# Kernel tuning notes

Measured on AMD Instinct MI355X. Metric: run time of the kernel, lower is better.

Reference implementation:

```python
import jax, jax.numpy as jnp
import numpy as np

B, T, IN = 32, 64, 90
U, SEG = 4, 16          # conductor steps, decoder steps per segment (T = U*SEG)
H1, HC, HD, Z = 2048, 1024, 1024, 512


def _lstm_layer(x, wih, whh, bih, bhh, h0=None, c0=None, reverse=False):
    """PyTorch-convention LSTM layer. x: [B,T,D]. Returns (ys [B,T,H], final h [B,H])."""
    b = x.shape[0]
    H = whh.shape[1]
    # precompute input projection for all timesteps: [T,B,4H]
    xp = jnp.swapaxes(jnp.einsum('btd,gd->btg', x, wih) + bih, 0, 1)
    if h0 is None:
        h0 = jnp.zeros((b, H), x.dtype)
        c0 = h0
    def step(carry, xt):
        h, c = carry
        g = xt + h @ whh.T + bhh
        i, f, gg, o = jnp.split(g, 4, axis=-1)  # torch gate order i,f,g,o
        c = jax.nn.sigmoid(f) * c + jax.nn.sigmoid(i) * jnp.tanh(gg)
        h = jax.nn.sigmoid(o) * jnp.tanh(c)
        return (h, c), h
    (h, c), ys = jax.lax.scan(step, (h0, c0), xp, reverse=reverse)
    return jnp.swapaxes(ys, 0, 1), h


def _cell(xin, h, c, wih, whh, bih, bhh):
    g = xin @ wih.T + bih + h @ whh.T + bhh
    i, f, gg, o = jnp.split(g, 4, axis=-1)
    c = jax.nn.sigmoid(f) * c + jax.nn.sigmoid(i) * jnp.tanh(gg)
    h = jax.nn.sigmoid(o) * jnp.tanh(c)
    return h, c


def setup_inputs() -> dict:
    key = jax.random.key(0)
    ks = iter(jax.random.split(key, 64))
    def p(*shape):
        return jax.random.normal(next(ks), shape, dtype=jnp.float32) * 0.02
    inp = {}
    inp['x'] = jax.random.normal(next(ks), (B, T, IN), dtype=jnp.float32)
    inp['eps'] = jax.random.normal(next(ks), (B, Z), dtype=jnp.float32)
    # encoder bi-LSTM: 2 layers x 2 directions
    for name, d in [('e0f', IN), ('e0b', IN), ('e1f', 2 * H1), ('e1b', 2 * H1)]:
        inp[name + '_wih'] = p(4 * H1, d)
        inp[name + '_whh'] = p(4 * H1, H1)
        inp[name + '_bih'] = p(4 * H1)
        inp[name + '_bhh'] = p(4 * H1)
    inp['wm'] = p(Z, 2 * H1); inp['bm'] = p(Z)
    inp['ws'] = p(Z, 2 * H1); inp['bs'] = p(Z)
    inp['w2'] = p(4 * HC, Z); inp['b2'] = p(4 * HC)
    # conductor LSTM: 2 layers, input size 1
    for name, d in [('c0', 1), ('c1', HC)]:
        inp[name + '_wih'] = p(4 * HC, d)
        inp[name + '_whh'] = p(4 * HC, HC)
        inp[name + '_bih'] = p(4 * HC)
        inp[name + '_bhh'] = p(4 * HC)
    inp['w3'] = p(4 * HD, HC); inp['b3'] = p(4 * HD)
    # two decoder LSTMCells
    for name, d in [('d1', HC + IN), ('d2', HD)]:
        inp[name + '_wih'] = p(4 * HD, d)
        inp[name + '_whh'] = p(4 * HD, HD)
        inp[name + '_bih'] = p(4 * HD)
        inp[name + '_bhh'] = p(4 * HD)
    inp['w4'] = p(IN, HD); inp['b4'] = p(IN)
    return inp


def reference(x, eps,
              e0f_wih, e0f_whh, e0f_bih, e0f_bhh,
              e0b_wih, e0b_whh, e0b_bih, e0b_bhh,
              e1f_wih, e1f_whh, e1f_bih, e1f_bhh,
              e1b_wih, e1b_whh, e1b_bih, e1b_bhh,
              wm, bm, ws, bs, w2, b2,
              c0_wih, c0_whh, c0_bih, c0_bhh,
              c1_wih, c1_whh, c1_bih, c1_bhh,
              w3, b3,
              d1_wih, d1_whh, d1_bih, d1_bhh,
              d2_wih, d2_whh, d2_bih, d2_bhh,
              w4, b4):
    b = x.shape[0]
    # ----- encode: 2-layer bidirectional LSTM, take layer-1 fwd/bwd final h -----
    y0f, _ = _lstm_layer(x, e0f_wih, e0f_whh, e0f_bih, e0f_bhh)
    y0b, _ = _lstm_layer(x, e0b_wih, e0b_whh, e0b_bih, e0b_bhh, reverse=True)
    y0 = jnp.concatenate([y0f, y0b], axis=2)  # [B,T,2*H1]
    _, hf = _lstm_layer(y0, e1f_wih, e1f_whh, e1f_bih, e1f_bhh)
    _, hb = _lstm_layer(y0, e1b_wih, e1b_whh, e1b_bih, e1b_bhh, reverse=True)
    ht = jnp.concatenate([hf, hb], axis=1)  # [B,4096]
    z_mean = ht @ wm.T + bm
    z_std = jnp.log1p(jnp.exp(ht @ ws.T + bs))  # softplus as in source
    z = z_mean + eps * z_std
    # ----- conductor -----
    t = jnp.tanh(z @ w2.T + b2)
    h1, h2, c1, c2 = jnp.split(t, 4, axis=1)  # source order: h1,h2,c1,c2
    zin = jnp.zeros((b, U, 1), x.dtype)
    yc0, _ = _lstm_layer(zin, c0_wih, c0_whh, c0_bih, c0_bhh, h1, c1)
    emb, _ = _lstm_layer(yc0, c1_wih, c1_whh, c1_bih, c1_bhh, h2, c2)  # [B,U,HC]
    def segment(prev, e):
        s = jnp.tanh(e @ w3.T + b3)
        sh1, sh2, sc1, sc2 = jnp.split(s, 4, axis=1)
        def step(carry, _):
            dh1, dc1, dh2, dc2, p = carry
            inp = jnp.concatenate([e, p], axis=1)
            dh1, dc1 = _cell(inp, dh1, dc1, d1_wih, d1_whh, d1_bih, d1_bhh)
            dh2, dc2 = _cell(dh1, dh2, dc2, d2_wih, d2_whh, d2_bih, d2_bhh)
            p = dh2 @ w4.T + b4
            return (dh1, dc1, dh2, dc2, p), p
        carry, outs = jax.lax.scan(step, (sh1, sc1, sh2, sc2, prev), None, length=SEG)
        return carry[4], outs  # outs: [SEG,B,IN]
    prev0 = jnp.zeros((b, IN), x.dtype)
    _, outs = jax.lax.scan(segment, prev0, jnp.swapaxes(emb, 0, 1))  # [U,SEG,B,IN]
    out = jnp.transpose(outs.reshape(U * SEG, b, IN), (1, 0, 2))  # [B,T,IN]
    out = jax.nn.softmax(out, axis=2)
    return out, z_mean, z_std
```

## Files before the change

kernel.cpp:

```cpp
#include <hip/hip_runtime.h>
#include <hip/hip_cooperative_groups.h>
#include <math.h>

#define BB 32
#define TT 64
#define INPW 90
#define NU 4
#define NH1 2048
#define NHC 1024
#define NHD 1024
#define NZ 512
#define BSTRIDE 12800

typedef unsigned short u16;
typedef __attribute__((ext_vector_type(8))) short short8;
typedef __attribute__((ext_vector_type(4))) float f32x4;
typedef __attribute__((ext_vector_type(4))) unsigned uv4;
typedef __attribute__((ext_vector_type(2))) unsigned uv2;

__device__ __forceinline__ float sigf(float v) { return 1.0f / (1.0f + __expf(-v)); }

__device__ __forceinline__ u16 f2bf(float f) {
  unsigned u = __float_as_uint(f);
  unsigned r = (u + 0x7FFFu + ((u >> 16) & 1u)) >> 16;
  return (u16)r;
}
__device__ __forceinline__ float bf2f(u16 b) { return __uint_as_float(((unsigned)b) << 16); }

__device__ __forceinline__ void cstore16(u16* p, uv4 v) {
  asm volatile("global_store_dwordx4 %0, %1, off sc0 sc1" :: "v"(p), "v"(v) : "memory");
}
__device__ __forceinline__ void cstore8(u16* p, uv2 v) {
  asm volatile("global_store_dwordx2 %0, %1, off sc0 sc1" :: "v"(p), "v"(v) : "memory");
}
__device__ __forceinline__ void cstore4(unsigned* p, unsigned v) {
  asm volatile("global_store_dword %0, %1, off sc0 sc1" :: "v"(p), "v"(v) : "memory");
}
__device__ __forceinline__ unsigned fload(const unsigned* p) {
  unsigned r;
  asm volatile("global_load_dword %0, %1, off sc0 sc1\n\ts_waitcnt vmcnt(0)"
               : "=v"(r) : "v"(p) : "memory");
  return r;
}
__device__ __forceinline__ void gbar(unsigned* base) {
  asm volatile("s_waitcnt vmcnt(0)" ::: "memory");
  __syncthreads();
  if (threadIdx.x == 0) {
    unsigned old = atomicAdd(&base[(blockIdx.x & 15) * 512], 1u);
    if (old == 15u) {
      unsigned m = atomicAdd(&base[16 * 512], 1u);
      if (m == 15u) {
#pragma unroll
        for (int k = 0; k < 8; ++k) cstore4(&base[(17 + k) * 512], 1u);
        asm volatile("s_waitcnt vmcnt(0)" ::: "memory");
      }
    }
    while (!fload(&base[(17 + (blockIdx.x & 7)) * 512])) __builtin_amdgcn_s_sleep(2);
  }
  __syncthreads();
}

__global__ void cvt_flat(const float* __restrict__ s, u16* __restrict__ d, long n) {
  long i = ((long)blockIdx.x * 256 + threadIdx.x) * 4;
  if (i >= n) return;
  float4 v = *(const float4*)&s[i];
  d[i] = f2bf(v.x); d[i + 1] = f2bf(v.y); d[i + 2] = f2bf(v.z); d[i + 3] = f2bf(v.w);
}

__global__ void cvt_pad(const float* __restrict__ s, int sld, int cols,
                        u16* __restrict__ d, int dld, int rows) {
  int c = blockIdx.x * blockDim.x + threadIdx.x;
  int r = blockIdx.y;
  if (c >= dld) return;
  d[(long)r * dld + c] = (c < cols) ? f2bf(s[(long)r * sld + c]) : (u16)0;
}

__global__ void xcvt(const float* __restrict__ x, u16* __restrict__ xb) {
  int r = blockIdx.x, c = threadIdx.x;
  int b = r & 31, t = r >> 5;
  float v = (c < INPW) ? x[((long)b * TT + t) * INPW + c] : 0.0f;
  xb[(long)r * 128 + c] = f2bf(v);
}

__global__ void w4t_k(const float* __restrict__ w4, u16* __restrict__ w4tb) {
  int k = blockIdx.x, n = threadIdx.x;
  w4tb[(long)k * 128 + n] = (n < INPW) ? f2bf(w4[(long)n * NHD + k]) : (u16)0;
}

__global__ void bfuse_k(const float* __restrict__ d1_wih, const float* __restrict__ b4,
                        float* __restrict__ bfuse) {
  int r = blockIdx.x * 256 + threadIdx.x;
  if (r >= 4096) return;
  float s = 0.0f;
  for (int n = 0; n < INPW; ++n) s += d1_wih[(long)r * 1114 + 1024 + n] * b4[n];
  bfuse[r] = s;
}

__global__ __launch_bounds__(256) void gemm_bf(
    const u16* __restrict__ A, int lda, const u16* __restrict__ Bw, int ldb,
    const float* __restrict__ bias, u16* __restrict__ C, int ldc, int K, int mode,
    int nbm, int nbn) {
  __shared__ u16 Asm[128 * 64];
  __shared__ u16 Bsm[128 * 64];
  const int tid = threadIdx.x;
  const int w = tid >> 6, q = (tid >> 4) & 3, ln = tid & 15;
  const int wm = w & 1, wn = w >> 1;
  int fid = blockIdx.x;
  int sidx = fid >> 3, xcd = fid & 7;
  int bm, bn;
  if ((nbm & 7) == 0) { bn = sidx % nbn; bm = xcd * (nbm >> 3) + sidx / nbn; }
  else if ((nbn & 7) == 0) { bm = sidx % nbm; bn = xcd * (nbn >> 3) + sidx / nbm; }
  else { bm = fid % nbm; bn = fid / nbm; }
  const long am0 = (long)bm * 128;
  const long bn0 = (long)bn * 128;
  f32x4 acc[4][4] = {};
  const int srow = tid >> 3, ssl = tid & 7;
  const u16* Ap = A + (am0 + srow) * lda + ssl * 8;
  const u16* Bp = Bw + (bn0 + srow) * ldb + ssl * 8;
  uint4 va[4], vb[4];
  int soff[4];
#pragma unroll
  for (int i = 0; i < 4; ++i) {
    va[i] = *(const uint4*)(Ap + (long)i * 32 * lda);
    vb[i] = *(const uint4*)(Bp + (long)i * 32 * ldb);
    int r = srow + i * 32;
    soff[i] = r * 64 + ((ssl ^ (r & 7)) << 3);
  }
  int k0 = 0;
  for (;;) {
    __syncthreads();
#pragma unroll
    for (int i = 0; i < 4; ++i) {
      *(uint4*)&Asm[soff[i]] = va[i];
      *(uint4*)&Bsm[soff[i]] = vb[i];
    }
    __syncthreads();
    k0 += 64;
    if (k0 < K) {
#pragma unroll
      for (int i = 0; i < 4; ++i) {
        va[i] = *(const uint4*)(Ap + k0 + (long)i * 32 * lda);
        vb[i] = *(const uint4*)(Bp + k0 + (long)i * 32 * ldb);
      }
    }
#pragma unroll
    for (int kh = 0; kh < 2; ++kh) {
      short8 af[4], bg[4];
#pragma unroll
      for (int t = 0; t < 4; ++t) {
        int arr = wm * 64 + t * 16 + ln;
        af[t] = *(short8*)&Asm[arr * 64 + (((q + 4 * kh) ^ (arr & 7)) << 3)];
        int brr = wn * 64 + t * 16 + ln;
        bg[t] = *(short8*)&Bsm[brr * 64 + (((q + 4 * kh) ^ (brr & 7)) << 3)];
      }
#pragma unroll
      for (int mt = 0; mt < 4; ++mt)
#pragma unroll
        for (int nt = 0; nt < 4; ++nt)
          acc[mt][nt] = __builtin_amdgcn_mfma_f32_16x16x32_bf16(af[mt], bg[nt], acc[mt][nt], 0, 0, 0);
    }
    if (k0 >= K) break;
  }
#pragma unroll
  for (int nt = 0; nt < 4; ++nt) {
    long n = bn0 + wn * 64 + nt * 16 + ln;
    float bv = bias ? bias[n] : 0.0f;
#pragma unroll
    for (int mt = 0; mt < 4; ++mt) {
#pragma unroll
      for (int r = 0; r < 4; ++r) {
        long m = am0 + wm * 64 + mt * 16 + (q << 2) + r;
        long dst;
        if (mode == 0) {
          dst = m * ldc + n;
        } else if (mode == 1) {
          long j = n & 2047, g = n >> 11;
          dst = (((m >> 5) * 256 + (j >> 3)) * 32 + (m & 31)) * 32 + (j & 7) * 4 + g;
        } else {
          long j = n & 1023, g = n >> 10;
          dst = ((j >> 2) * 128 + m) * 16 + (j & 3) * 4 + g;
        }
        C[dst] = f2bf(acc[mt][nt][r] + bv);
      }
    }
  }
}

__global__ __launch_bounds__(256) void gemm128(
    const float* __restrict__ A, int lda, const float* __restrict__ W, int ldw,
    const float* __restrict__ bias, float* __restrict__ C, int ldc,
    int M, int K, int act, u16* __restrict__ Cb) {
  __shared__ float As[16][132];
  __shared__ float Bs[16][132];
  const int tid = threadIdx.x;
  const int bm = blockIdx.x, bn = blockIdx.y;
  const int tm = tid & 15, tn = tid >> 4;
  float acc[8][8] = {};
  for (int k0 = 0; k0 < K; k0 += 16) {
#pragma unroll
    for (int it = 0; it < 2; ++it) {
      int e = it * 256 + tid;
      int r = e >> 2, c4 = (e & 3) * 4;
      int m = bm * 128 + r;
      float4 v = make_float4(0.f, 0.f, 0.f, 0.f);
      if (m < M) v = *(const float4*)&A[(long)m * lda + k0 + c4];
      As[c4 + 0][r] = v.x; As[c4 + 1][r] = v.y; As[c4 + 2][r] = v.z; As[c4 + 3][r] = v.w;
      int n = bn * 128 + r;
      float4 w = *(const float4*)&W[(long)n * ldw + k0 + c4];
      Bs[c4 + 0][r] = w.x; Bs[c4 + 1][r] = w.y; Bs[c4 + 2][r] = w.z; Bs[c4 + 3][r] = w.w;
    }
    __syncthreads();
#pragma unroll
    for (int kk = 0; kk < 16; ++kk) {
      float4 a0 = *(const float4*)&As[kk][tm * 8];
      float4 a1 = *(const float4*)&As[kk][tm * 8 + 4];
      float4 b0 = *(const float4*)&Bs[kk][tn * 8];
      float4 b1 = *(const float4*)&Bs[kk][tn * 8 + 4];
      float av[8] = {a0.x, a0.y, a0.z, a0.w, a1.x, a1.y, a1.z, a1.w};
      float bv[8] = {b0.x, b0.y, b0.z, b0.w, b1.x, b1.y, b1.z, b1.w};
#pragma unroll
      for (int i = 0; i < 8; ++i)
#pragma unroll
        for (int j = 0; j < 8; ++j)
          acc[i][j] += av[i] * bv[j];
    }
    __syncthreads();
  }
#pragma unroll
  for (int i = 0; i < 8; ++i) {
    int m = bm * 128 + tm * 8 + i;
    if (m >= M) continue;
#pragma unroll
    for (int j = 0; j < 8; ++j) {
      int n = bn * 128 + tn * 8 + j;
      float v = acc[i][j] + bias[n];
      if (act == 1) v = tanhf(v);
      else if (act == 2) v = log1pf(__expf(v));
      C[(long)m * ldc + n] = v;
      if (Cb) Cb[(long)m * ldc + n] = f2bf(v);
    }
  }
}

__global__ __launch_bounds__(256) void latgemm(
    const float* __restrict__ A, const float* __restrict__ W,
    const float* __restrict__ bias, float* __restrict__ C, int act) {
  __shared__ float red[16][16][32];
  const int tid = threadIdx.x;
  const int c = tid & 15, ksl = tid >> 4;
  const int n = blockIdx.x * 16 + c;
  const float* wp = W + (long)n * 4096 + ksl * 256;
  const float* ap = A + ksl * 256;
  float acc[32];
#pragma unroll
  for (int r = 0; r < 32; ++r) acc[r] = 0.f;
  for (int k = 0; k < 256; k += 4) {
    float4 wv = *(const float4*)(wp + k);
#pragma unroll
    for (int r = 0; r < 32; ++r) {
      float4 hv = *(const float4*)(ap + (long)r * 4096 + k);
      acc[r] += hv.x * wv.x + hv.y * wv.y + hv.z * wv.z + hv.w * wv.w;
    }
  }
#pragma unroll
  for (int r = 0; r < 32; ++r) red[ksl][c][r] = acc[r];
  __syncthreads();
  for (int o = tid; o < 512; o += 256) {
    int cc = o >> 5, r = o & 31;
    float s = 0.f;
#pragma unroll
    for (int p = 0; p < 16; ++p) s += red[p][cc][r];
    s += bias[blockIdx.x * 16 + cc];
    if (act == 2) s = log1pf(__expf(s));
    C[(long)r * 512 + blockIdx.x * 16 + cc] = s;
  }
}

__global__ void zcalc_kernel(const float* __restrict__ zm, const float* __restrict__ zs,
                             const float* __restrict__ eps, float* __restrict__ z) {
  int e = blockIdx.x * 256 + threadIdx.x;
  if (e < BB * NZ) z[e] = zm[e] + eps[e] * zs[e];
}

__global__ void softmax_kernel(float* __restrict__ out) {
  long row = blockIdx.x;
  float* p = out + row * INPW;
  int lane = threadIdx.x;
  float v0 = (lane < INPW) ? p[lane] : -1e30f;
  float v1 = (lane + 64 < INPW) ? p[lane + 64] : -1e30f;
  float m = fmaxf(v0, v1);
#pragma unroll
  for (int off = 32; off > 0; off >>= 1) m = fmaxf(m, __shfl_xor(m, off));
  float e0 = (lane < INPW) ? __expf(v0 - m) : 0.0f;
  float e1 = (lane + 64 < INPW) ? __expf(v1 - m) : 0.0f;
  float sum = e0 + e1;
#pragma unroll
  for (int off = 32; off > 0; off >>= 1) sum += __shfl_xor(sum, off);
  float inv = 1.0f / sum;
  if (lane < INPW) p[lane] = e0 * inv;
  if (lane + 64 < INPW) p[lane + 64] = e1 * inv;
}

struct EncArgs {
  const u16* whh[2];
  const u16* xp[2];
  const float* bhh[2];
  u16* y0b;
  u16* h1a[2];
  float* htb;
  unsigned* bar;
  int layer;
};

__global__ __launch_bounds__(512) void enc_coop(EncArgs A) {
  __shared__ u16 Wl[2 * 64 * 64 * 8];
  __shared__ __align__(16) float red[4 * 64 * 4];
  __shared__ __align__(16) u16 hstage[32][8];
  const int tid = threadIdx.x;
  const int w = tid >> 6, l = tid & 63;
  const int rt = w & 1, bh = (w >> 1) & 1, kh = w >> 2;
  const int kg = l >> 4, b0 = l & 15;
  const int j0 = blockIdx.x * 8;
  const int jout = j0 + rt * 4 + kg;
  const int batch = bh * 16 + b0;
  float* redp = &red[((bh * 2 + rt) * 64 + l) * 4];

  for (int dir = 0; dir < 2; ++dir) {
    __syncthreads();
    {
      const u16* W = A.whh[dir];
      for (int e = tid; e < 8192; e += 512) {
        int ert = e >> 12, es = (e >> 6) & 63, el = e & 63;
        int etr = el & 15;
        long gr = (long)(etr & 3) * 2048 + j0 + ert * 4 + (etr >> 2);
        *(uint4*)&Wl[((ert * 64 + es) * 64 + el) * 8] =
            *(const uint4*)&W[gr * 2048 + (el >> 4) * 8 + (long)es * 32];
      }
    }
    __syncthreads();
    const float* bhh = A.bhh[dir];
    const u16* xp = A.xp[dir];
    const float bi0 = bhh[jout], bi1 = bhh[2048 + jout],
                bi2 = bhh[4096 + jout], bi3 = bhh[6144 + jout];
    float creg = 0.f;
    ushort4 xv4 = make_ushort4(0, 0, 0, 0);
    if (kh == 0) {
      int tt0 = dir ? 63 : 0;
      xv4 = *(const ushort4*)(xp + ((((long)tt0 * 256 + blockIdx.x) * 32 + batch) * 32)
                              + (rt * 4 + kg) * 4);
    }
    for (int s = 0; s < 64; ++s) {
      if (s) gbar(A.bar + (long)(dir * 63 + (s - 1)) * BSTRIDE);
      const int tt = dir ? 63 - s : s;
      f32x4 acc = {0.f, 0.f, 0.f, 0.f};
      if (s) {
        const u16* hb; long hld;
        if (A.layer == 0) {
          int tp = dir ? tt + 1 : tt - 1;
          hb = A.y0b + (long)tp * 32 * 4096 + dir * 2048;
          hld = 4096;
        } else {
          hb = A.h1a[dir] + (long)(s - 1) * 32 * 2048;
          hld = 2048;
        }
        const u16* xv = hb + (long)batch * hld + kg * 8;
        for (int ks = kh * 32; ks < kh * 32 + 32; ks += 8) {
          uint4 bv[8]; short8 av[8];
#pragma unroll
          for (int uu = 0; uu < 8; ++uu)
            bv[uu] = *(const uint4*)(xv + (long)(ks + uu) * 32);
#pragma unroll
          for (int uu = 0; uu < 8; ++uu)
            av[uu] = *(const short8*)&Wl[((rt * 64 + ks + uu) * 64 + l) * 8];
#pragma unroll
          for (int uu = 0; uu < 8; ++uu)
            acc = __builtin_amdgcn_mfma_f32_16x16x32_bf16(av[uu], *(short8*)&bv[uu], acc, 0, 0, 0);
        }
      }
      if (kh) *(f32x4*)redp = acc;
      __syncthreads();
      if (kh == 0) {
        f32x4 o = *(f32x4*)redp;
        float g0 = acc[0] + o[0] + bi0 + bf2f(xv4.x);
        float g1 = acc[1] + o[1] + bi1 + bf2f(xv4.y);
        float g2 = acc[2] + o[2] + bi2 + bf2f(xv4.z);
        float g3 = acc[3] + o[3] + bi3 + bf2f(xv4.w);
        float iv = sigf(g0), fv = sigf(g1), gv = tanhf(g2), ov = sigf(g3);
        float c = fv * creg + iv * gv;
        creg = c;
        float h = ov * tanhf(c);
        hstage[batch][rt * 4 + kg] = f2bf(h);
        if (A.layer == 1 && s == 63) A.htb[batch * 4096 + dir * 2048 + jout] = h;
      }
      __syncthreads();
      if (tid < 32) {
        uv4 v = *(const uv4*)&hstage[tid][0];
        u16* dst;
        if (A.layer == 0) dst = &A.y0b[((long)tt * 32 + tid) * 4096 + dir * 2048 + j0];
        else dst = &A.h1a[dir][((long)s * 32 + tid) * 2048 + j0];
        cstore16(dst, v);
      }
      if (kh == 0 && s < 63) {
        int ttn = dir ? 62 - s : s + 1;
        xv4 = *(const ushort4*)(xp + ((((long)ttn * 256 + blockIdx.x) * 32 + batch) * 32)
                                + (rt * 4 + kg) * 4);
      }
    }
  }
}

__device__ __forceinline__ void stage_w1024(u16* Wl, int m, const u16* W, int j0, int tid) {
  for (int e = tid; e < 2048; e += 512) {
    int kh = e >> 10, s = (e >> 6) & 15, el = e & 63;
    int tr = el & 15;
    long gr = (long)(tr & 3) * 1024 + j0 + (tr >> 2);
    *(uint4*)&Wl[(((m * 2 + kh) * 16 + s) * 64 + el) * 8] =
        *(const uint4*)&W[gr * 1024 + kh * 512 + (el >> 4) * 8 + s * 32];
  }
}

__device__ __forceinline__ void cell1024_lds(
    const u16* Wl, int m0, int m1,
    int j0, int tid, float* red, u16* hstage,
    const u16* X0, long x0ld,
    const u16* X1, long x1ld,
    float xg0, float xg1, float xg2, float xg3,
    float b0, float b1, float b2, float b3,
    float co, float* crp,
    u16* hout, long hld, float* houtf, long hfld) {
  const int w = tid >> 6, l = tid & 63;
  const int bh = w & 1, kh = w >> 1;
  const int kg = l >> 4;
  const int koff = kh * 256 + kg * 8;
  const int batch = bh * 16 + (l & 15);
  const int sbase = (kh >> 1) * 16 + (kh & 1) * 8;
  const int jout = j0 + kg;
  f32x4 acc = {0.f, 0.f, 0.f, 0.f};
  if (X0) {
    const u16* xpt = X0 + (long)batch * x0ld + koff;
    const int sb = m0 * 32 + sbase;
    uint4 bv[8]; short8 av[8];
#pragma unroll
    for (int uu = 0; uu < 8; ++uu) bv[uu] = *(const uint4*)(xpt + (long)uu * 32);
#pragma unroll
    for (int uu = 0; uu < 8; ++uu) av[uu] = *(const short8*)&Wl[((sb + uu) * 64 + l) * 8];
#pragma unroll
    for (int uu = 0; uu < 8; ++uu)
      acc = __builtin_amdgcn_mfma_f32_16x16x32_bf16(av[uu], *(short8*)&bv[uu], acc, 0, 0, 0);
  }
  if (X1) {
    const u16* xpt = X1 + (long)batch * x1ld + koff;
    const int sb = m1 * 32 + sbase;
    uint4 bv[8]; short8 av[8];
#pragma unroll
    for (int uu = 0; uu < 8; ++uu) bv[uu] = *(const uint4*)(xpt + (long)uu * 32);
#pragma unroll
    for (int uu = 0; uu < 8; ++uu) av[uu] = *(const short8*)&Wl[((sb + uu) * 64 + l) * 8];
#pragma unroll
    for (int uu = 0; uu < 8; ++uu)
      acc = __builtin_amdgcn_mfma_f32_16x16x32_bf16(av[uu], *(short8*)&bv[uu], acc, 0, 0, 0);
  }
  if (kh) *(f32x4*)&red[((kh - 1) * 2 + bh) * 256 + l * 4] = acc;
  __syncthreads();
  if (kh == 0) {
#pragma unroll
    for (int p = 0; p < 3; ++p) {
      f32x4 o = *(f32x4*)&red[(p * 2 + bh) * 256 + l * 4];
      acc[0] += o[0]; acc[1] += o[1]; acc[2] += o[2]; acc[3] += o[3];
    }
    float g0 = acc[0] + b0 + xg0;
    float g1 = acc[1] + b1 + xg1;
    float g2 = acc[2] + b2 + xg2;
    float g3 = acc[3] + b3 + xg3;
    float iv = sigf(g0), fv = sigf(g1), gv = tanhf(g2), ov = sigf(g3);
    float c = fv * co + iv * gv;
    *crp = c;
    float h = ov * tanhf(c);
    hstage[batch * 4 + kg] = f2bf(h);
    if (houtf) houtf[(long)batch * hfld + jout] = h;
  }
  __syncthreads();
  if (tid < 32) {
    uv2 v = *(const uv2*)&hstage[tid * 4];
    cstore8(&hout[(long)tid * hld + j0], v);
  }
}

struct CondArgs {
  const u16 *c0h, *c1w, *c1h, *tvecb;
  const float* tvec;
  u16 *yc0b, *embb;
  float* embf;
  const float *b0i, *b0h, *b1i, *b1h;
  unsigned* bar;
};
__global__ __launch_bounds__(512) void cond_coop(CondArgs A) {
  __shared__ u16 Wl[3 * 32 * 512];
  __shared__ __align__(16) float red[6 * 256];
  __shared__ __align__(16) u16 hstage[128];
  const int j0 = blockIdx.x * 4;
  const int tid = threadIdx.x;
  const int w = tid >> 6, l = tid & 63;
  const int bh = w & 1;
  const int jout = j0 + (l >> 4);
  const int batch = bh * 16 + (l & 15);
  stage_w1024(Wl, 0, A.c0h, j0, tid);
  stage_w1024(Wl, 1, A.c1w, j0, tid);
  stage_w1024(Wl, 2, A.c1h, j0, tid);
  const float cb00 = A.b0i[jout] + A.b0h[jout];
  const float cb01 = A.b0i[1024 + jout] + A.b0h[1024 + jout];
  const float cb02 = A.b0i[2048 + jout] + A.b0h[2048 + jout];
  const float cb03 = A.b0i[3072 + jout] + A.b0h[3072 + jout];
  const float cb10 = A.b1i[jout] + A.b1h[jout];
  const float cb11 = A.b1i[1024 + jout] + A.b1h[1024 + jout];
  const float cb12 = A.b1i[2048 + jout] + A.b1h[2048 + jout];
  const float cb13 = A.b1i[3072 + jout] + A.b1h[3072 + jout];
  const float c0init = A.tvec[2048 + (long)batch * 4096 + jout];
  const float c1init = A.tvec[3072 + (long)batch * 4096 + jout];
  __syncthreads();
  float cr0 = c0init, cr1 = c1init;
  int bi = 0;
  for (int u = 0; u < NU; ++u) {
    cell1024_lds(Wl, 0, -1, j0, tid, red, hstage,
                 u ? A.yc0b + (long)(u - 1) * 32 * 1024 : A.tvecb, u ? 1024 : 4096,
                 nullptr, 0,
                 0.f, 0.f, 0.f, 0.f,
                 cb00, cb01, cb02, cb03,
                 cr0, &cr0,
                 A.yc0b + (long)u * 32 * 1024, 1024, nullptr, 0);
    gbar(A.bar + (long)(bi++) * BSTRIDE);
    cell1024_lds(Wl, 1, 2, j0, tid, red, hstage,
                 A.yc0b + (long)u * 32 * 1024, 1024,
                 u ? A.embb + (long)(u - 1) * 32 * 1024 : A.tvecb + 1024, u ? 1024 : 4096,
                 0.f, 0.f, 0.f, 0.f,
                 cb10, cb11, cb12, cb13,
                 cr1, &cr1,
                 A.embb + (long)u * 32 * 1024, 1024, A.embf + (long)u * 32 * 1024, 1024);
    if (u < NU - 1) gbar(A.bar + (long)(bi++) * BSTRIDE);
  }
}

struct DecArgs {
  const u16 *d1h, *wfuse, *d2w, *d2h, *xeb, *sallb;
  const float* sall;
  u16 *dh1all, *dh2all;
  const float *bfuse, *b1h, *b2i, *b2h;
  unsigned* bar;
};
__global__ __launch_bounds__(512) void dec_coop(DecArgs A) {
  __shared__ u16 Wl[4 * 32 * 512];
  __shared__ __align__(16) float red[6 * 256];
  __shared__ __align__(16) u16 hstage[128];
  const int j0 = blockIdx.x * 4;
  const int tid = threadIdx.x;
  const int w = tid >> 6, l = tid & 63;
  const int bh = w & 1;
  const int kg = l >> 4;
  const int jout = j0 + kg;
  const int batch = bh * 16 + (l & 15);
  stage_w1024(Wl, 0, A.d1h, j0, tid);
  stage_w1024(Wl, 1, A.wfuse, j0, tid);
  stage_w1024(Wl, 2, A.d2w, j0, tid);
  stage_w1024(Wl, 3, A.d2h, j0, tid);
  const float b1z0 = A.b1h[jout], b1z1 = A.b1h[1024 + jout],
              b1z2 = A.b1h[2048 + jout], b1z3 = A.b1h[3072 + jout];
  const float b1n0 = b1z0 + A.bfuse[jout], b1n1 = b1z1 + A.bfuse[1024 + jout],
              b1n2 = b1z2 + A.bfuse[2048 + jout], b1n3 = b1z3 + A.bfuse[3072 + jout];
  const float b20 = A.b2i[jout] + A.b2h[jout];
  const float b21 = A.b2i[1024 + jout] + A.b2h[1024 + jout];
  const float b22 = A.b2i[2048 + jout] + A.b2h[2048 + jout];
  const float b23 = A.b2i[3072 + jout] + A.b2h[3072 + jout];
  const u16* xqb = A.xeb + (long)blockIdx.x * 128 * 16;
  ushort4 xq4 = *(const ushort4*)(xqb + (long)batch * 16 + kg * 4);
  float con1 = A.sall[(long)batch * 4096 + 2048 + jout];
  float con2 = A.sall[(long)batch * 4096 + 3072 + jout];
  __syncthreads();
  float cr1 = 0.f, cr2 = 0.f;
  int bi = 0;
  for (int t = 0; t < TT; ++t) {
    const int u = t >> 4, sg = t & 15;
    if (sg == 0) { cr1 = con1; cr2 = con2; }
    cell1024_lds(Wl, 0, 1, j0, tid, red, hstage,
                 sg ? A.dh1all + (long)(t - 1) * 32 * 1024 : A.sallb + (long)u * 32 * 4096,
                 sg ? 1024 : 4096,
                 t ? A.dh2all + (long)(t - 1) * 32 * 1024 : nullptr, 1024,
                 bf2f(xq4.x), bf2f(xq4.y), bf2f(xq4.z), bf2f(xq4.w),
                 t ? b1n0 : b1z0, t ? b1n1 : b1z1, t ? b1n2 : b1z2, t ? b1n3 : b1z3,
                 cr1, &cr1,
                 A.dh1all + (long)t * 32 * 1024, 1024, nullptr, 0);
    gbar(A.bar + (long)(bi++) * BSTRIDE);
    cell1024_lds(Wl, 2, 3, j0, tid, red, hstage,
                 A.dh1all + (long)t * 32 * 1024, 1024,
                 sg ? A.dh2all + (long)(t - 1) * 32 * 1024 : A.sallb + (long)u * 32 * 4096 + 1024,
                 sg ? 1024 : 4096,
                 0.f, 0.f, 0.f, 0.f,
                 b20, b21, b22, b23,
                 cr2, &cr2,
                 A.dh2all + (long)t * 32 * 1024, 1024, nullptr, 0);
    if (sg == 15 && u < 3) {
      xq4 = *(const ushort4*)(xqb + (long)(u + 1) * 32 * 16 + (long)batch * 16 + kg * 4);
      con1 = A.sall[(long)(u + 1) * 32 * 4096 + (long)batch * 4096 + 2048 + jout];
      con2 = A.sall[(long)(u + 1) * 32 * 4096 + (long)batch * 4096 + 3072 + jout];
    }
    if (t < TT - 1) gbar(A.bar + (long)(bi++) * BSTRIDE);
  }
}

__global__ __launch_bounds__(256) void proj_all(const u16* __restrict__ dh2all,
                                                const u16* __restrict__ w4b,
                                                const float* __restrict__ b4,
                                                float* __restrict__ out) {
  __shared__ u16 hs[8 * 1024];
  const int r0 = blockIdx.x * 8;
  for (int e = threadIdx.x; e < 1024; e += 256)
    ((uint4*)hs)[e] = ((const uint4*)(dh2all + (long)r0 * 1024))[e];
  __syncthreads();
  for (int o = threadIdx.x; o < 8 * INPW; o += 256) {
    int rr = o / INPW, n = o % INPW;
    const u16* wr = w4b + (long)n * 1024;
    const u16* hr = hs + rr * 1024;
    float s = 0.0f;
    for (int k = 0; k < 1024; ++k) s += bf2f(hr[k]) * bf2f(wr[k]);
    int row = r0 + rr;
    int tt = row >> 5, b = row & 31;
    out[((long)b * TT + tt) * INPW + n] = s + b4[n];
  }
}

extern "C" void kernel_launch(void* const* d_in, const int* in_sizes, int n_in,
                              void* d_out, int out_size, void* d_ws, size_t ws_size,
                              hipStream_t stream) {
  (void)in_sizes; (void)n_in; (void)out_size;
  const float* x        = (const float*)d_in[0];
  const float* eps      = (const float*)d_in[1];
  const float* e0f_wih  = (const float*)d_in[2];
  const float* e0f_whh  = (const float*)d_in[3];
  const float* e0f_bih  = (const float*)d_in[4];
  const float* e0f_bhh  = (const float*)d_in[5];
  const float* e0b_wih  = (const float*)d_in[6];
  const float* e0b_whh  = (const float*)d_in[7];
  const float* e0b_bih  = (const float*)d_in[8];
  const float* e0b_bhh  = (const float*)d_in[9];
  const float* e1f_wih  = (const float*)d_in[10];
  const float* e1f_whh  = (const float*)d_in[11];
  const float* e1f_bih  = (const float*)d_in[12];
  const float* e1f_bhh  = (const float*)d_in[13];
  const float* e1b_wih  = (const float*)d_in[14];
  const float* e1b_whh  = (const float*)d_in[15];
  const float* e1b_bih  = (const float*)d_in[16];
  const float* e1b_bhh  = (const float*)d_in[17];
  const float* wm  = (const float*)d_in[18];
  const float* bm  = (const float*)d_in[19];
  const float* wsw = (const float*)d_in[20];
  const float* bsv = (const float*)d_in[21];
  const float* w2  = (const float*)d_in[22];
  const float* b2  = (const float*)d_in[23];
  const float* c0_whh = (const float*)d_in[25];
  const float* c0_bih = (const float*)d_in[26];
  const float* c0_bhh = (const float*)d_in[27];
  const float* c1_wih = (const float*)d_in[28];
  const float* c1_whh = (const float*)d_in[29];
  const float* c1_bih = (const float*)d_in[30];
  const float* c1_bhh = (const float*)d_in[31];
  const float* w3 = (const float*)d_in[32];
  const float* b3 = (const float*)d_in[33];
  const float* d1_wih = (const float*)d_in[34];
  const float* d1_whh = (const float*)d_in[35];
  const float* d1_bih = (const float*)d_in[36];
  const float* d1_bhh = (const float*)d_in[37];
  const float* d2_wih = (const float*)d_in[38];
  const float* d2_whh = (const float*)d_in[39];
  const float* d2_bih = (const float*)d_in[40];
  const float* d2_bhh = (const float*)d_in[41];
  const float* w4 = (const float*)d_in[42];
  const float* b4 = (const float*)d_in[43];

  float* out = (float*)d_out;
  float* zm_out = out + (size_t)BB * TT * INPW;
  float* zs_out = zm_out + BB * NZ;

  char* wbase = (char*)d_ws;
  size_t cur = 0;
  auto AL = [&](size_t bytes) -> void* {
    void* p = wbase + cur;
    cur = (cur + bytes + 255) & ~(size_t)255;
    return p;
  };
  u16* xb    = (u16*)AL(2048L * 128 * 2);
  u16* e0wf  = (u16*)AL(8192L * 128 * 2);
  u16* e0wb  = (u16*)AL(8192L * 128 * 2);
  u16* e0hf  = (u16*)AL(8192L * 2048 * 2);
  u16* e0hb  = (u16*)AL(8192L * 2048 * 2);
  u16* e1wf  = (u16*)AL(8192L * 4096 * 2);
  u16* e1wb  = (u16*)AL(8192L * 4096 * 2);
  u16* e1hf  = (u16*)AL(8192L * 2048 * 2);
  u16* e1hb  = (u16*)AL(8192L * 2048 * 2);
  u16* c0h   = (u16*)AL(4096L * 1024 * 2);
  u16* c1w   = (u16*)AL(4096L * 1024 * 2);
  u16* c1h   = (u16*)AL(4096L * 1024 * 2);
  u16* d1we  = (u16*)AL(4096L * 1024 * 2);
  u16* d1wp  = (u16*)AL(4096L * 128 * 2);
  u16* d1h   = (u16*)AL(4096L * 1024 * 2);
  u16* d2w   = (u16*)AL(4096L * 1024 * 2);
  u16* d2h   = (u16*)AL(4096L * 1024 * 2);
  u16* w4b   = (u16*)AL(90L * 1024 * 2);
  u16* w4tb  = (u16*)AL(1024L * 128 * 2);
  u16* wfuse = (u16*)AL(4096L * 1024 * 2);
  float* bfuse = (float*)AL(4096L * 4);
  u16* xp0f  = (u16*)AL(2048L * 8192 * 2);
  u16* xp0b  = (u16*)AL(2048L * 8192 * 2);
  u16* y0b   = (u16*)AL(2048L * 4096 * 2);
  u16* xp1f  = (u16*)AL(2048L * 8192 * 2);
  u16* xp1b  = (u16*)AL(2048L * 8192 * 2);
  u16* h1af  = (u16*)AL(64L * 32 * 2048 * 2);
  u16* h1ab  = (u16*)AL(64L * 32 * 2048 * 2);
  u16* tvecb = (u16*)AL(32L * 4096 * 2);
  u16* yc0b  = (u16*)AL(4L * 32 * 1024 * 2);
  u16* embb  = (u16*)AL(4L * 32 * 1024 * 2);
  u16* sallb = (u16*)AL(128L * 4096 * 2);
  u16* xeb   = (u16*)AL(128L * 4096 * 2);
  u16* dh1all= (u16*)AL(64L * 32 * 1024 * 2);
  u16* dh2all= (u16*)AL(64L * 32 * 1024 * 2);
  float* htb  = (float*)AL(32L * 4096 * 4);
  float* zbuf = (float*)AL(32L * 512 * 4);
  float* tvec = (float*)AL(32L * 4096 * 4);
  float* embf = (float*)AL(128L * 1024 * 4);
  float* sall = (float*)AL(128L * 4096 * 4);
  unsigned* barp = (unsigned*)AL(400L * BSTRIDE * 4);
  if (cur > ws_size) return;

  unsigned* bar_enc0 = barp;
  unsigned* bar_enc1 = barp + 128L * BSTRIDE;
  unsigned* bar_cond = barp + 256L * BSTRIDE;
  unsigned* bar_dec  = barp + 264L * BSTRIDE;

  auto cf = [&](const float* s, u16* d, long n) {
    cvt_flat<<<dim3((unsigned)((n / 4 + 255) / 256)), 256, 0, stream>>>(s, d, n);
  };
  cf(e0f_whh, e0hf, 8192L * 2048);
  cf(e0b_whh, e0hb, 8192L * 2048);
  cf(e1f_wih, e1wf, 8192L * 4096);
  cf(e1b_wih, e1wb, 8192L * 4096);
  cf(e1f_whh, e1hf, 8192L * 2048);
  cf(e1b_whh, e1hb, 8192L * 2048);
  cf(c0_whh, c0h, 4096L * 1024);
  cf(c1_wih, c1w, 4096L * 1024);
  cf(c1_whh, c1h, 4096L * 1024);
  cf(d1_whh, d1h, 4096L * 1024);
  cf(d2_wih, d2w, 4096L * 1024);
  cf(d2_whh, d2h, 4096L * 1024);
  cf(w4, w4b, 90L * 1024);
  cvt_pad<<<dim3(1, 8192), 128, 0, stream>>>(e0f_wih, 90, 90, e0wf, 128, 8192);
  cvt_pad<<<dim3(1, 8192), 128, 0, stream>>>(e0b_wih, 90, 90, e0wb, 128, 8192);
  cvt_pad<<<dim3(4, 4096), 256, 0, stream>>>(d1_wih, 1114, 1024, d1we, 1024, 4096);
  cvt_pad<<<dim3(1, 4096), 128, 0, stream>>>(d1_wih + 1024, 1114, 90, d1wp, 128, 4096);
  xcvt<<<dim3(2048), 128, 0, stream>>>(x, xb);
  w4t_k<<<dim3(1024), 128, 0, stream>>>(w4, w4tb);
  bfuse_k<<<dim3(16), 256, 0, stream>>>(d1_wih, b4, bfuse);
  hipMemsetAsync(barp, 0, 400L * BSTRIDE * 4, stream);

  gemm_bf<<<dim3(256), 256, 0, stream>>>(d1wp, 128, w4tb, 128, nullptr, wfuse, 1024, 128, 0, 32, 8);
  gemm_bf<<<dim3(1024), 256, 0, stream>>>(xb, 128, e0wf, 128, e0f_bih, xp0f, 8192, 128, 1, 16, 64);
  gemm_bf<<<dim3(1024), 256, 0, stream>>>(xb, 128, e0wb, 128, e0b_bih, xp0b, 8192, 128, 1, 16, 64);

  {
    EncArgs ea{};
    ea.whh[0] = e0hf; ea.whh[1] = e0hb;
    ea.xp[0] = xp0f; ea.xp[1] = xp0b;
    ea.bhh[0] = e0f_bhh; ea.bhh[1] = e0b_bhh;
    ea.y0b = y0b; ea.h1a[0] = h1af; ea.h1a[1] = h1ab; ea.htb = htb;
    ea.bar = bar_enc0; ea.layer = 0;
    void* args[] = {&ea};
    (void)hipLaunchCooperativeKernel((void*)enc_coop, dim3(256), dim3(512), args, 0, stream);
  }

  gemm_bf<<<dim3(1024), 256, 0, stream>>>(y0b, 4096, e1wf, 4096, e1f_bih, xp1f, 8192, 4096, 1, 16, 64);
  gemm_bf<<<dim3(1024), 256, 0, stream>>>(y0b, 4096, e1wb, 4096, e1b_bih, xp1b, 8192, 4096, 1, 16, 64);

  {
    EncArgs ea{};
    ea.whh[0] = e1hf; ea.whh[1] = e1hb;
    ea.xp[0] = xp1f; ea.xp[1] = xp1b;
    ea.bhh[0] = e1f_bhh; ea.bhh[1] = e1b_bhh;
    ea.y0b = y0b; ea.h1a[0] = h1af; ea.h1a[1] = h1ab; ea.htb = htb;
    ea.bar = bar_enc1; ea.layer = 1;
    void* args[] = {&ea};
    (void)hipLaunchCooperativeKernel((void*)enc_coop, dim3(256), dim3(512), args, 0, stream);
  }

  latgemm<<<dim3(32), 256, 0, stream>>>(htb, wm, bm, zm_out, 0);
  latgemm<<<dim3(32), 256, 0, stream>>>(htb, wsw, bsv, zs_out, 2);
  zcalc_kernel<<<dim3(64), 256, 0, stream>>>(zm_out, zs_out, eps, zbuf);
  gemm128<<<dim3(1, 32), 256, 0, stream>>>(zbuf, 512, w2, 512, b2, tvec, 4096, 32, 512, 1, tvecb);

  {
    CondArgs ca{};
    ca.c0h = c0h; ca.c1w = c1w; ca.c1h = c1h;
    ca.tvecb = tvecb; ca.tvec = tvec;
    ca.yc0b = yc0b; ca.embb = embb; ca.embf = embf;
    ca.b0i = c0_bih; ca.b0h = c0_bhh; ca.b1i = c1_bih; ca.b1h = c1_bhh;
    ca.bar = bar_cond;
    void* args[] = {&ca};
    (void)hipLaunchCooperativeKernel((void*)cond_coop, dim3(256), dim3(512), args, 0, stream);
  }

  gemm128<<<dim3(1, 32), 256, 0, stream>>>(embf, 1024, w3, 1024, b3, sall, 4096, 128, 1024, 1, sallb);
  gemm_bf<<<dim3(32), 256, 0, stream>>>(embb, 1024, d1we, 1024, d1_bih, xeb, 4096, 1024, 2, 1, 32);

  {
    DecArgs da{};
    da.d1h = d1h; da.wfuse = wfuse; da.d2w = d2w; da.d2h = d2h;
    da.xeb = xeb; da.sallb = sallb; da.sall = sall;
    da.dh1all = dh1all; da.dh2all = dh2all;
    da.bfuse = bfuse; da.b1h = d1_bhh; da.b2i = d2_bih; da.b2h = d2_bhh;
    da.bar = bar_dec;
    void* args[] = {&da};
    (void)hipLaunchCooperativeKernel((void*)dec_coop, dim3(256), dim3(512), args, 0, stream);
  }

  proj_all<<<dim3(256), 256, 0, stream>>>(dh2all, w4b, b4, out);
  softmax_kernel<<<dim3(BB * TT), 64, 0, stream>>>(out);
}
```

Baseline: 6.000 ms.

## Double-buffer gemm_bf via direct global-to-LDS loads and pre-permute gate rows

```diff
diff --git a/kernel.cpp b/kernel.cpp
--- a/kernel.cpp
+++ b/kernel.cpp
@@ -60,6 +60,12 @@
   __syncthreads();
 }
 
+__device__ __forceinline__ void gload16(const u16* g, u16* l) {
+  __builtin_amdgcn_global_load_lds(
+      (const __attribute__((address_space(1))) unsigned*)g,
+      (__attribute__((address_space(3))) unsigned*)l, 16, 0, 0);
+}
+
 __global__ void cvt_flat(const float* __restrict__ s, u16* __restrict__ d, long n) {
   long i = ((long)blockIdx.x * 256 + threadIdx.x) * 4;
   if (i >= n) return;
@@ -73,6 +79,21 @@
   int r = blockIdx.y;
   if (c >= dld) return;
   d[(long)r * dld + c] = (c < cols) ? f2bf(s[(long)r * sld + c]) : (u16)0;
+}
+
+__global__ void cvt_permrow(const float* __restrict__ s, int sld, int cols,
+                            u16* __restrict__ d, int dld, int H) {
+  int c = blockIdx.x * blockDim.x + threadIdx.x;
+  int r = blockIdx.y;
+  if (c >= dld) return;
+  long sr = (long)(r & 3) * H + (r >> 2);
+  d[(long)r * dld + c] = (c < cols) ? f2bf(s[sr * sld + c]) : (u16)0;
+}
+
+__global__ void bias_perm(const float* __restrict__ s, float* __restrict__ d, int H) {
+  int n = blockIdx.x * 256 + threadIdx.x;
+  if (n >= 4 * H) return;
+  d[n] = s[(long)(n & 3) * H + (n >> 2)];
 }
 
 __global__ void xcvt(const float* __restrict__ x, u16* __restrict__ xb) {
@@ -100,10 +121,10 @@
     const u16* __restrict__ A, int lda, const u16* __restrict__ Bw, int ldb,
     const float* __restrict__ bias, u16* __restrict__ C, int ldc, int K, int mode,
     int nbm, int nbn) {
-  __shared__ u16 Asm[128 * 64];
-  __shared__ u16 Bsm[128 * 64];
+  __shared__ u16 Asm[2][128 * 64];
+  __shared__ u16 Bsm[2][128 * 64];
   const int tid = threadIdx.x;
-  const int w = tid >> 6, q = (tid >> 4) & 3, ln = tid & 15;
+  const int w = tid >> 6, l = tid & 63, q = (tid >> 4) & 3, ln = tid & 15;
   const int wm = w & 1, wn = w >> 1;
   int fid = blockIdx.x;
   int sidx = fid >> 3, xcd = fid & 7;
@@ -113,45 +134,36 @@
   else { bm = fid % nbm; bn = fid / nbm; }
   const long am0 = (long)bm * 128;
   const long bn0 = (long)bn * 128;
+  const u16* Ap0 = A + am0 * lda;
+  const u16* Bp0 = Bw + bn0 * ldb;
   f32x4 acc[4][4] = {};
-  const int srow = tid >> 3, ssl = tid & 7;
-  const u16* Ap = A + (am0 + srow) * lda + ssl * 8;
-  const u16* Bp = Bw + (bn0 + srow) * ldb + ssl * 8;
-  uint4 va[4], vb[4];
-  int soff[4];
-#pragma unroll
-  for (int i = 0; i < 4; ++i) {
-    va[i] = *(const uint4*)(Ap + (long)i * 32 * lda);
-    vb[i] = *(const uint4*)(Bp + (long)i * 32 * ldb);
-    int r = srow + i * 32;
-    soff[i] = r * 64 + ((ssl ^ (r & 7)) << 3);
-  }
-  int k0 = 0;
-  for (;;) {
-    __syncthreads();
+
+  auto stage = [&](int b, int k0) {
 #pragma unroll
     for (int i = 0; i < 4; ++i) {
-      *(uint4*)&Asm[soff[i]] = va[i];
-      *(uint4*)&Bsm[soff[i]] = vb[i];
-    }
-    __syncthreads();
-    k0 += 64;
-    if (k0 < K) {
-#pragma unroll
-      for (int i = 0; i < 4; ++i) {
-        va[i] = *(const uint4*)(Ap + k0 + (long)i * 32 * lda);
-        vb[i] = *(const uint4*)(Bp + k0 + (long)i * 32 * ldb);
-      }
-    }
+      int row = (w * 4 + i) * 8 + (l >> 3);
+      int col = (((l & 7) ^ (row & 7)) << 3) + k0;
+      gload16(Ap0 + (long)row * lda + col, &Asm[b][(w * 4 + i) * 512]);
+      gload16(Bp0 + (long)row * ldb + col, &Bsm[b][(w * 4 + i) * 512]);
+    }
+  };
+
+  const int kt = K >> 6;
+  stage(0, 0);
+  asm volatile("s_waitcnt vmcnt(0)" ::: "memory");
+  __syncthreads();
+  int buf = 0;
+  for (int t = 0; t < kt; ++t) {
+    if (t + 1 < kt) stage(buf ^ 1, (t + 1) << 6);
 #pragma unroll
     for (int kh = 0; kh < 2; ++kh) {
       short8 af[4], bg[4];
 #pragma unroll
-      for (int t = 0; t < 4; ++t) {
-        int arr = wm * 64 + t * 16 + ln;
-        af[t] = *(short8*)&Asm[arr * 64 + (((q + 4 * kh) ^ (arr & 7)) << 3)];
-        int brr = wn * 64 + t * 16 + ln;
-        bg[t] = *(short8*)&Bsm[brr * 64 + (((q + 4 * kh) ^ (brr & 7)) << 3)];
+      for (int tt2 = 0; tt2 < 4; ++tt2) {
+        int arr = wm * 64 + tt2 * 16 + ln;
+        af[tt2] = *(short8*)&Asm[buf][arr * 64 + (((q + 4 * kh) ^ (arr & 7)) << 3)];
+        int brr = wn * 64 + tt2 * 16 + ln;
+        bg[tt2] = *(short8*)&Bsm[buf][brr * 64 + (((q + 4 * kh) ^ (brr & 7)) << 3)];
       }
 #pragma unroll
       for (int mt = 0; mt < 4; ++mt)
@@ -159,7 +171,9 @@
         for (int nt = 0; nt < 4; ++nt)
           acc[mt][nt] = __builtin_amdgcn_mfma_f32_16x16x32_bf16(af[mt], bg[nt], acc[mt][nt], 0, 0, 0);
     }
-    if (k0 >= K) break;
+    asm volatile("s_waitcnt vmcnt(0)" ::: "memory");
+    __syncthreads();
+    buf ^= 1;
   }
 #pragma unroll
   for (int nt = 0; nt < 4; ++nt) {
@@ -174,11 +188,9 @@
         if (mode == 0) {
           dst = m * ldc + n;
         } else if (mode == 1) {
-          long j = n & 2047, g = n >> 11;
-          dst = (((m >> 5) * 256 + (j >> 3)) * 32 + (m & 31)) * 32 + (j & 7) * 4 + g;
+          dst = (((m >> 5) * 256 + (n >> 5)) * 32 + (m & 31)) * 32 + (n & 31);
         } else {
-          long j = n & 1023, g = n >> 10;
-          dst = ((j >> 2) * 128 + m) * 16 + (j & 3) * 4 + g;
+          dst = ((n >> 4) * 128 + m) * 16 + (n & 15);
         }
         C[dst] = f2bf(acc[mt][nt][r] + bv);
       }
@@ -707,6 +719,11 @@
   u16* w4tb  = (u16*)AL(1024L * 128 * 2);
   u16* wfuse = (u16*)AL(4096L * 1024 * 2);
   float* bfuse = (float*)AL(4096L * 4);
+  float* pb_e0f = (float*)AL(8192L * 4);
+  float* pb_e0b = (float*)AL(8192L * 4);
+  float* pb_e1f = (float*)AL(8192L * 4);
+  float* pb_e1b = (float*)AL(8192L * 4);
+  float* pb_d1  = (float*)AL(4096L * 4);
   u16* xp0f  = (u16*)AL(2048L * 8192 * 2);
   u16* xp0b  = (u16*)AL(2048L * 8192 * 2);
   u16* y0b   = (u16*)AL(2048L * 4096 * 2);
@@ -739,8 +756,6 @@
   };
   cf(e0f_whh, e0hf, 8192L * 2048);
   cf(e0b_whh, e0hb, 8192L * 2048);
-  cf(e1f_wih, e1wf, 8192L * 4096);
-  cf(e1b_wih, e1wb, 8192L * 4096);
   cf(e1f_whh, e1hf, 8192L * 2048);
   cf(e1b_whh, e1hb, 8192L * 2048);
   cf(c0_whh, c0h, 4096L * 1024);
@@ -750,9 +765,16 @@
   cf(d2_wih, d2w, 4096L * 1024);
   cf(d2_whh, d2h, 4096L * 1024);
   cf(w4, w4b, 90L * 1024);
-  cvt_pad<<<dim3(1, 8192), 128, 0, stream>>>(e0f_wih, 90, 90, e0wf, 128, 8192);
-  cvt_pad<<<dim3(1, 8192), 128, 0, stream>>>(e0b_wih, 90, 90, e0wb, 128, 8192);
-  cvt_pad<<<dim3(4, 4096), 256, 0, stream>>>(d1_wih, 1114, 1024, d1we, 1024, 4096);
+  cvt_permrow<<<dim3(1, 8192), 128, 0, stream>>>(e0f_wih, 90, 90, e0wf, 128, 2048);
+  cvt_permrow<<<dim3(1, 8192), 128, 0, stream>>>(e0b_wih, 90, 90, e0wb, 128, 2048);
+  cvt_permrow<<<dim3(16, 8192), 256, 0, stream>>>(e1f_wih, 4096, 4096, e1wf, 4096, 2048);
+  cvt_permrow<<<dim3(16, 8192), 256, 0, stream>>>(e1b_wih, 4096, 4096, e1wb, 4096, 2048);
+  cvt_permrow<<<dim3(4, 4096), 256, 0, stream>>>(d1_wih, 1114, 1024, d1we, 1024, 1024);
+  bias_perm<<<dim3(32), 256, 0, stream>>>(e0f_bih, pb_e0f, 2048);
+  bias_perm<<<dim3(32), 256, 0, stream>>>(e0b_bih, pb_e0b, 2048);
+  bias_perm<<<dim3(32), 256, 0, stream>>>(e1f_bih, pb_e1f, 2048);
+  bias_perm<<<dim3(32), 256, 0, stream>>>(e1b_bih, pb_e1b, 2048);
+  bias_perm<<<dim3(16), 256, 0, stream>>>(d1_bih, pb_d1, 1024);
   cvt_pad<<<dim3(1, 4096), 128, 0, stream>>>(d1_wih + 1024, 1114, 90, d1wp, 128, 4096);
   xcvt<<<dim3(2048), 128, 0, stream>>>(x, xb);
   w4t_k<<<dim3(1024), 128, 0, stream>>>(w4, w4tb);
@@ -760,8 +782,8 @@
   hipMemsetAsync(barp, 0, 400L * BSTRIDE * 4, stream);
 
   gemm_bf<<<dim3(256), 256, 0, stream>>>(d1wp, 128, w4tb, 128, nullptr, wfuse, 1024, 128, 0, 32, 8);
-  gemm_bf<<<dim3(1024), 256, 0, stream>>>(xb, 128, e0wf, 128, e0f_bih, xp0f, 8192, 128, 1, 16, 64);
-  gemm_bf<<<dim3(1024), 256, 0, stream>>>(xb, 128, e0wb, 128, e0b_bih, xp0b, 8192, 128, 1, 16, 64);
+  gemm_bf<<<dim3(1024), 256, 0, stream>>>(xb, 128, e0wf, 128, pb_e0f, xp0f, 8192, 128, 1, 16, 64);
+  gemm_bf<<<dim3(1024), 256, 0, stream>>>(xb, 128, e0wb, 128, pb_e0b, xp0b, 8192, 128, 1, 16, 64);
 
   {
     EncArgs ea{};
@@ -774,8 +796,8 @@
     (void)hipLaunchCooperativeKernel((void*)enc_coop, dim3(256), dim3(512), args, 0, stream);
   }
 
-  gemm_bf<<<dim3(1024), 256, 0, stream>>>(y0b, 4096, e1wf, 4096, e1f_bih, xp1f, 8192, 4096, 1, 16, 64);
-  gemm_bf<<<dim3(1024), 256, 0, stream>>>(y0b, 4096, e1wb, 4096, e1b_bih, xp1b, 8192, 4096, 1, 16, 64);
+  gemm_bf<<<dim3(1024), 256, 0, stream>>>(y0b, 4096, e1wf, 4096, pb_e1f, xp1f, 8192, 4096, 1, 16, 64);
+  gemm_bf<<<dim3(1024), 256, 0, stream>>>(y0b, 4096, e1wb, 4096, pb_e1b, xp1b, 8192, 4096, 1, 16, 64);
 
   {
     EncArgs ea{};
@@ -805,7 +827,7 @@
   }
 
   gemm128<<<dim3(1, 32), 256, 0, stream>>>(embf, 1024, w3, 1024, b3, sall, 4096, 128, 1024, 1, sallb);
-  gemm_bf<<<dim3(32), 256, 0, stream>>>(embb, 1024, d1we, 1024, d1_bih, xeb, 4096, 1024, 2, 1, 32);
+  gemm_bf<<<dim3(32), 256, 0, stream>>>(embb, 1024, d1we, 1024, pb_d1, xeb, 4096, 1024, 2, 1, 32);
 
   {
     DecArgs da{};
```

Measured after the change: 4.900 ms. -18.3%, faster.
